# Performance work log

Measured on AMD Instinct MI355X. Metric: run time of the kernel, lower is better.

## Reference

```python
import jax, jax.numpy as jnp
import numpy as np

D_MODEL = 512
N_HEADS = 8
HEAD_DIM = D_MODEL // N_HEADS
B, T = 128, 256


def setup_inputs() -> dict:
    key = jax.random.key(0)
    ks = jax.random.split(key, 5)
    s = 1.0 / np.sqrt(D_MODEL)
    return {
        "x": jax.random.normal(ks[0], (B, T, D_MODEL), dtype=jnp.float32),
        "W_qkv": jax.random.uniform(ks[1], (D_MODEL, 3 * D_MODEL), jnp.float32, -s, s),
        "b_qkv": jax.random.uniform(ks[2], (3 * D_MODEL,), jnp.float32, -s, s),
        "W_out": jax.random.uniform(ks[3], (D_MODEL, D_MODEL), jnp.float32, -s, s),
        "b_out": jax.random.uniform(ks[4], (D_MODEL,), jnp.float32, -s, s),
    }


def reference(x, W_qkv, b_qkv, W_out, b_out):
    Bsz, Tlen, C = x.shape
    H, hd = N_HEADS, HEAD_DIM
    qkv = x @ W_qkv + b_qkv                       # [B,T,3C]
    qkv = qkv.reshape(Bsz, Tlen, 3, H, hd).transpose(2, 0, 3, 1, 4)  # [3,B,H,T,hd]
    q, k, v = qkv[0], qkv[1], qkv[2]
    att = jnp.einsum('bhtd,bhsd->bhts', q, k) * (1.0 / np.sqrt(hd))  # [B,H,T,T]
    causal = jnp.tril(jnp.ones((Tlen, Tlen), dtype=bool))
    att = jnp.where(causal, att, -jnp.inf)
    att = jax.nn.softmax(att, axis=-1)
    y = jnp.einsum('bhts,bhsd->bhtd', att, v)     # [B,H,T,hd]
    y = y.transpose(0, 2, 1, 3).reshape(Bsz, Tlen, C)
    return y @ W_out + b_out
```

## Files before the change

### kernel.cpp

```cpp
#include <hip/hip_runtime.h>
#include <hip/hip_bf16.h>

typedef __attribute__((ext_vector_type(4))) float f32x4;
typedef __attribute__((ext_vector_type(8))) short s16x8;
typedef unsigned short u16;

__device__ __forceinline__ u16 f2bf(float f) {
    union { float f; unsigned int u; } a; a.f = f;
    unsigned int u = a.u;
    unsigned int lsb = (u >> 16) & 1u;
    u += 0x7fffu + lsb;
    return (u16)(u >> 16);
}

__device__ __forceinline__ void gll16(const u16* g, u16* l) {
    __builtin_amdgcn_global_load_lds(
        (const __attribute__((address_space(1))) unsigned int*)g,
        (__attribute__((address_space(3))) unsigned int*)l, 16, 0, 0);
}


__global__ __launch_bounds__(256) void cvt_all_kernel(const float* __restrict__ x,
                                                      const float* __restrict__ W_qkv,
                                                      const float* __restrict__ W_out,
                                                      u16* __restrict__ xb,
                                                      u16* __restrict__ WqkvT,
                                                      u16* __restrict__ WoutT) {
    int bid = blockIdx.x;
    if (bid < 16384) {
        int i = bid * 256 + threadIdx.x;
        float4 v = ((const float4*)x)[i];
        ushort4 o;
        o.x = f2bf(v.x); o.y = f2bf(v.y); o.z = f2bf(v.z); o.w = f2bf(v.w);
        ((ushort4*)xb)[i] = o;
    } else if (bid < 16768) {
        int id = (bid - 16384) * 256 + threadIdx.x;
        int n = id % 1536, kg = id / 1536;
        union { u16 h[8]; int4 v; } o;
#pragma unroll
        for (int e = 0; e < 8; ++e) o.h[e] = f2bf(W_qkv[(kg * 8 + e) * 1536 + n]);
        *(int4*)&WqkvT[n * 512 + kg * 8] = o.v;
    } else {
        int id = (bid - 16768) * 256 + threadIdx.x;
        int n = id % 512, kg = id / 512;
        union { u16 h[8]; int4 v; } o;
#pragma unroll
        for (int e = 0; e < 8; ++e) o.h[e] = f2bf(W_out[(kg * 8 + e) * 512 + n]);
        *(int4*)&WoutT[n * 512 + kg * 8] = o.v;
    }
}


template<int K>
__device__ __forceinline__ void stage256(const u16* __restrict__ A, const u16* __restrict__ Bt,
                                         int m0, int n0, int kt, u16* As, u16* Bs) {
    const int lane = threadIdx.x & 63, w = threadIdx.x >> 6;
    const int lr = lane >> 3;
    const int lg = lane & 7;
    const int sgA = lg ^ lr;
#pragma unroll
    for (int j = 0; j < 4; ++j) {
        const int blk = w * 4 + j;
        gll16(&A[(m0 + blk * 8 + lr) * K + kt + sgA * 8], &As[blk * 512]);
    }
#pragma unroll
    for (int j = 0; j < 4; ++j) {
        const int blk = w * 4 + j;
        const int sgB = lg ^ ((2 * j + (lr >> 2)) & 7);
        gll16(&Bt[(n0 + blk * 8 + lr) * K + kt + sgB * 8], &Bs[blk * 512]);
    }
}

template<int K>
__device__ __forceinline__ void gemm_tile256(const u16* __restrict__ A, const u16* __restrict__ Bt,
                                             int m0, int n0,
                                             u16* As0, u16* Bs0, u16* As1, u16* Bs1,
                                             f32x4 (&acc)[8][4]) {
    const int lane = threadIdx.x & 63, li = lane & 15, quad = lane >> 4;
    const int w = threadIdx.x >> 6;
    const int wr = w >> 2, wc = w & 3;
    const int sw = li & 7;

    stage256<K>(A, Bt, m0, n0, 0, As0, Bs0);
    __syncthreads();

#pragma unroll
    for (int kt = 0; kt < K / 64; ++kt) {
        u16* Asc = (kt & 1) ? As1 : As0;
        u16* Bsc = (kt & 1) ? Bs1 : Bs0;
        if (kt + 1 < K / 64)
            stage256<K>(A, Bt, m0, n0, (kt + 1) * 64,
                        (kt & 1) ? As0 : As1, (kt & 1) ? Bs0 : Bs1);
#pragma unroll
        for (int kc = 0; kc < 2; ++kc) {
            s16x8 af[8], bf[4];
#pragma unroll
            for (int i = 0; i < 8; ++i)
                af[i] = *(const s16x8*)&Asc[(wr * 128 + i * 16 + li) * 64 + (((quad + kc * 4) ^ sw)) * 8];
#pragma unroll
            for (int j = 0; j < 4; ++j)
                bf[j] = *(const s16x8*)&Bsc[(wc * 64 + li * 4 + j) * 64 + (((quad + kc * 4) ^ sw)) * 8];
#pragma unroll
            for (int i = 0; i < 8; ++i)
#pragma unroll
                for (int j = 0; j < 4; ++j)
                    acc[i][j] = __builtin_amdgcn_mfma_f32_16x16x32_bf16(af[i], bf[j], acc[i][j], 0, 0, 0);
        }
        __syncthreads();
    }
}


__global__ __launch_bounds__(512, 2) void gemm_qkv_kernel(const u16* __restrict__ xb,
                                                          const u16* __restrict__ WqkvT,
                                                          const float* __restrict__ b_qkv,
                                                          u16* __restrict__ Qb, u16* __restrict__ Kb,
                                                          u16* __restrict__ Vtb) {
    __shared__ __align__(16) u16 S[69632];
    u16* As0 = S;          u16* Bs0 = S + 16384;
    u16* As1 = S + 32768;  u16* Bs1 = S + 49152;

    f32x4 acc[8][4];
#pragma unroll
    for (int i = 0; i < 8; ++i)
#pragma unroll
        for (int j = 0; j < 4; ++j) acc[i][j] = {0.f, 0.f, 0.f, 0.f};

    const int id = blockIdx.x, xcd = id & 7, slot = id >> 3;
    const int mt = xcd * 16 + slot / 6, nt = slot % 6;
    const int m0 = mt * 256, n0 = nt * 256;
    gemm_tile256<512>(xb, WqkvT, m0, n0, As0, Bs0, As1, Bs1, acc);

    const int lane = threadIdx.x & 63, li = lane & 15, quad = lane >> 4;
    const int w = threadIdx.x >> 6, wr = w >> 2, wc = w & 3;
    const int c0 = n0 + wc * 64;
    float4 b4 = *(const float4*)&b_qkv[c0 + li * 4];

    if (n0 < 1024) {
        const int which = c0 >> 9, hh = (c0 >> 6) & 7;
        u16* __restrict__ dst = which ? Kb : Qb;
#pragma unroll
        for (int i = 0; i < 8; ++i)
#pragma unroll
            for (int r = 0; r < 4; ++r) {
                int row = m0 + wr * 128 + i * 16 + quad * 4 + r;
                int bb = row >> 8, tt = row & 255;
                int bh = (bb * 8 + hh) << 14;
                ushort4 o;
                o.x = f2bf(acc[i][0][r] + b4.x); o.y = f2bf(acc[i][1][r] + b4.y);
                o.z = f2bf(acc[i][2][r] + b4.z); o.w = f2bf(acc[i][3][r] + b4.w);
                *(ushort4*)&dst[bh + tt * 64 + li * 4] = o;
            }
    } else {
        u16* Rw = S + w * 8704;
#pragma unroll
        for (int i = 0; i < 8; ++i)
#pragma unroll
            for (int r = 0; r < 4; ++r) {
                int rl = i * 16 + quad * 4 + r;
                ushort4 o;
                o.x = f2bf(acc[i][0][r] + b4.x); o.y = f2bf(acc[i][1][r] + b4.y);
                o.z = f2bf(acc[i][2][r] + b4.z); o.w = f2bf(acc[i][3][r] + b4.w);
                *(ushort4*)&Rw[rl * 68 + li * 4] = o;
            }
        __syncthreads();
        const int hh = ((n0 >> 6) + wc) & 7;
        const size_t bh = ((size_t)(mt * 8 + hh)) << 14;
#pragma unroll
        for (int c = 0; c < 16; ++c) {
            int g = c * 64 + lane;
            int group = g >> 8;
            int d = (g & 255) >> 2;
            int sl8 = (g & 3) * 8;
            union { u16 h[8]; int4 v; } o;
#pragma unroll
            for (int e = 0; e < 8; ++e) o.h[e] = Rw[(group * 32 + sl8 + e) * 68 + d];
            *(int4*)&Vtb[bh + (wr * 4 + group) * 2048 + d * 32 + sl8] = o.v;
        }
    }
}


__global__ __launch_bounds__(512, 2) void gemm_out_kernel(const u16* __restrict__ Yb,
                                                          const u16* __restrict__ WoutT,
                                                          const float* __restrict__ b_out,
                                                          float* __restrict__ out) {
    __shared__ __align__(16) u16 As0[256 * 64];
    __shared__ __align__(16) u16 Bs0[256 * 64];
    __shared__ __align__(16) u16 As1[256 * 64];
    __shared__ __align__(16) u16 Bs1[256 * 64];
    f32x4 acc[8][4];
#pragma unroll
    for (int i = 0; i < 8; ++i)
#pragma unroll
        for (int j = 0; j < 4; ++j) acc[i][j] = {0.f, 0.f, 0.f, 0.f};

    const int id = blockIdx.x, xcd = id & 7, slot = id >> 3;
    const int mt = xcd * 16 + (slot >> 1), nt = slot & 1;
    const int m0 = mt * 256, n0 = nt * 256;
    gemm_tile256<512>(Yb, WoutT, m0, n0, As0, Bs0, As1, Bs1, acc);

    const int lane = threadIdx.x & 63, li = lane & 15, quad = lane >> 4;
    const int w = threadIdx.x >> 6, wr = w >> 2, wc = w & 3;
    const int c0 = n0 + wc * 64;
    float4 b4 = *(const float4*)&b_out[c0 + li * 4];

#pragma unroll
    for (int i = 0; i < 8; ++i)
#pragma unroll
        for (int r = 0; r < 4; ++r) {
            int row = m0 + wr * 128 + i * 16 + quad * 4 + r;
            float4 o;
            o.x = acc[i][0][r] + b4.x; o.y = acc[i][1][r] + b4.y;
            o.z = acc[i][2][r] + b4.z; o.w = acc[i][3][r] + b4.w;
            *(float4*)&out[row * 512 + c0 + li * 4] = o;
        }
}


__global__ __launch_bounds__(256, 2) void attn_kernel(const u16* __restrict__ Qb,
                                                      const u16* __restrict__ Kb,
                                                      const u16* __restrict__ Vtb,
                                                      u16* __restrict__ Yb) {
    __shared__ __align__(16) u16 Ks[256 * 64];
    __shared__ __align__(16) u16 pl[4 * 2 * 16 * 40];

    const int tid = threadIdx.x, wave = tid >> 6, lane = tid & 63, li = lane & 15, quad = lane >> 4;
    const int bhid = blockIdx.x;
    const int b = bhid >> 3, h = bhid & 7;
    const int bh = bhid << 14;

    s16x8 qf0 = *(const s16x8*)&Qb[bh + (wave * 16 + li) * 64 + quad * 8];
    s16x8 qf1 = *(const s16x8*)&Qb[bh + (wave * 16 + li) * 64 + 32 + quad * 8];

    {
        const int lr = lane >> 3;
        const int sg = (lane & 7) ^ lr;
#pragma unroll
        for (int j = 0; j < 8; ++j) {
            int blk = wave * 8 + j;
            gll16(&Kb[bh + (blk * 8 + lr) * 64 + sg * 8], &Ks[blk * 512]);
        }
    }
    __syncthreads();

    u16* plw = &pl[wave * 1280];

    for (int p = 0; p < 4; ++p) {
        const int qt = p * 4 + wave;
        const int qrb = qt * 16;
        const int nst = qt + 1;

        f32x4 sacc[16];
#pragma unroll
        for (int st = 0; st < 16; ++st) sacc[st] = {0.f, 0.f, 0.f, 0.f};
        const int sw = li & 7;
#pragma unroll
        for (int g = 0; g < 4; ++g) {
            if (g * 4 < nst) {
                s16x8 kf[4][2];
#pragma unroll
                for (int t = 0; t < 4; ++t) {
                    if (g * 4 + t < nst) {
                        int rb = ((g * 4 + t) * 16 + li) * 64;
                        kf[t][0] = *(const s16x8*)&Ks[rb + ((quad    ) ^ sw) * 8];
                        kf[t][1] = *(const s16x8*)&Ks[rb + ((quad + 4) ^ sw) * 8];
                    }
                }
#pragma unroll
                for (int t = 0; t < 4; ++t) {
                    if (g * 4 + t < nst) {
                        sacc[g*4+t] = __builtin_amdgcn_mfma_f32_16x16x32_bf16(qf0, kf[t][0], sacc[g*4+t], 0, 0, 0);
                        sacc[g*4+t] = __builtin_amdgcn_mfma_f32_16x16x32_bf16(qf1, kf[t][1], sacc[g*4+t], 0, 0, 0);
                    }
                }
            }
        }

        s16x8 nqf0 = qf0, nqf1 = qf1;
        if (p < 3) {
            int nqrb = ((p + 1) * 4 + wave) * 16;
            nqf0 = *(const s16x8*)&Qb[bh + (nqrb + li) * 64 + quad * 8];
            nqf1 = *(const s16x8*)&Qb[bh + (nqrb + li) * 64 + 32 + quad * 8];
        }

        float mx[4] = {-3e38f, -3e38f, -3e38f, -3e38f};
#pragma unroll
        for (int st = 0; st < 16; ++st) {
            if (st < nst) {
                int sg2 = st * 16 + li;
#pragma unroll
                for (int r = 0; r < 4; ++r) {
                    int tg = qrb + quad * 4 + r;
                    float v = (sg2 <= tg) ? sacc[st][r] * 0.125f : -3e38f;
                    sacc[st][r] = v;
                    mx[r] = fmaxf(mx[r], v);
                }
            }
        }
#pragma unroll
        for (int d = 1; d < 16; d <<= 1)
#pragma unroll
            for (int r = 0; r < 4; ++r) mx[r] = fmaxf(mx[r], __shfl_xor(mx[r], d, 64));

        const int ns32 = (nst + 1) >> 1;
        float l[4] = {0.f, 0.f, 0.f, 0.f};
        f32x4 oacc[4];
#pragma unroll
        for (int dt = 0; dt < 4; ++dt) oacc[dt] = {0.f, 0.f, 0.f, 0.f};

        s16x8 vf[2][4];
#pragma unroll
        for (int dt = 0; dt < 4; ++dt)
            vf[0][dt] = *(const s16x8*)&Vtb[bh + (li * 4 + dt) * 32 + quad * 8];

#pragma unroll
        for (int c = 0; c < 8; ++c) {
            if (c < ns32) {
                if (c + 1 < ns32) {
#pragma unroll
                    for (int dt = 0; dt < 4; ++dt)
                        vf[(c + 1) & 1][dt] = *(const s16x8*)&Vtb[bh + (c + 1) * 2048 + (li * 4 + dt) * 32 + quad * 8];
                }
                u16* pb = plw + (c & 1) * 640;
#pragma unroll
                for (int half = 0; half < 2; ++half) {
                    int st = c * 2 + half;
#pragma unroll
                    for (int r = 0; r < 4; ++r) {
                        float e = (st < nst) ? __expf(sacc[st][r] - mx[r]) : 0.f;
                        l[r] += e;
                        pb[(quad * 4 + r) * 40 + half * 16 + li] = f2bf(e);
                    }
                }
                s16x8 pf = *(const s16x8*)&pb[li * 40 + quad * 8];
#pragma unroll
                for (int dt = 0; dt < 4; ++dt)
                    oacc[dt] = __builtin_amdgcn_mfma_f32_16x16x32_bf16(pf, vf[c & 1][dt], oacc[dt], 0, 0, 0);
            }
        }

#pragma unroll
        for (int d = 1; d < 16; d <<= 1)
#pragma unroll
            for (int r = 0; r < 4; ++r) l[r] += __shfl_xor(l[r], d, 64);

#pragma unroll
        for (int r = 0; r < 4; ++r) {
            int tg = qrb + quad * 4 + r;
            float inv = 1.0f / l[r];
            ushort4 o;
            o.x = f2bf(oacc[0][r] * inv); o.y = f2bf(oacc[1][r] * inv);
            o.z = f2bf(oacc[2][r] * inv); o.w = f2bf(oacc[3][r] * inv);
            *(ushort4*)&Yb[(b * 256 + tg) * 512 + h * 64 + li * 4] = o;
        }

        qf0 = nqf0; qf1 = nqf1;
    }
}


extern "C" void kernel_launch(void* const* d_in, const int* in_sizes, int n_in,
                              void* d_out, int out_size, void* d_ws, size_t ws_size,
                              hipStream_t stream) {
    const float* x     = (const float*)d_in[0];
    const float* W_qkv = (const float*)d_in[1];
    const float* b_qkv = (const float*)d_in[2];
    const float* W_out = (const float*)d_in[3];
    const float* b_out = (const float*)d_in[4];
    float* out = (float*)d_out;

    char* ws = (char*)d_ws;
    u16* Qb    = (u16*)(ws);
    u16* Kb    = (u16*)(ws + 33554432);
    u16* Vtb   = (u16*)(ws + 67108864);
    u16* WqkvT = (u16*)(ws + 100663296);
    u16* WoutT = (u16*)(ws + 102236160);
    u16* xb    = (u16*)(ws + 102760448);
    u16* Yb    = xb;
    if (ws_size < (size_t)136314880) return;

    cvt_all_kernel<<<16896, 256, 0, stream>>>(x, W_qkv, W_out, xb, WqkvT, WoutT);
    gemm_qkv_kernel<<<768, 512, 0, stream>>>(xb, WqkvT, b_qkv, Qb, Kb, Vtb);
    attn_kernel<<<1024, 256, 0, stream>>>(Qb, Kb, Vtb, Yb);
    gemm_out_kernel<<<256, 512, 0, stream>>>(Yb, WoutT, b_out, out);
}
```

Before: 263.0 us.

## Single-buffer GEMM LDS, halve out-GEMM tile, balance attention and drop softmax max

The shared GEMM tile drops double buffering, halving LDS, and launch bounds go to 4 blocks per CU so more blocks can be resident. The QKV epilogue transposes V in two halves to fit the smaller LDS. The output GEMM moves to 128x256 tiles with twice as many blocks. The attention kernel interleaves query tiles per wave to balance causal work, and removes the running-max subtraction in softmax, exponentiating scaled scores directly. That risks overflow for large logits and loses load/compute overlap in the GEMMs.

```diff
diff --git a/kernel.cpp b/kernel.cpp
--- a/kernel.cpp
+++ b/kernel.cpp
@@ -55,8 +55,7 @@
 __device__ __forceinline__ void stage256(const u16* __restrict__ A, const u16* __restrict__ Bt,
                                          int m0, int n0, int kt, u16* As, u16* Bs) {
     const int lane = threadIdx.x & 63, w = threadIdx.x >> 6;
-    const int lr = lane >> 3;
-    const int lg = lane & 7;
+    const int lr = lane >> 3, lg = lane & 7;
     const int sgA = lg ^ lr;
 #pragma unroll
     for (int j = 0; j < 4; ++j) {
@@ -71,35 +70,29 @@
     }
 }
 
+
 template<int K>
 __device__ __forceinline__ void gemm_tile256(const u16* __restrict__ A, const u16* __restrict__ Bt,
-                                             int m0, int n0,
-                                             u16* As0, u16* Bs0, u16* As1, u16* Bs1,
+                                             int m0, int n0, u16* As, u16* Bs,
                                              f32x4 (&acc)[8][4]) {
     const int lane = threadIdx.x & 63, li = lane & 15, quad = lane >> 4;
     const int w = threadIdx.x >> 6;
     const int wr = w >> 2, wc = w & 3;
     const int sw = li & 7;
 
-    stage256<K>(A, Bt, m0, n0, 0, As0, Bs0);
-    __syncthreads();
-
 #pragma unroll
     for (int kt = 0; kt < K / 64; ++kt) {
-        u16* Asc = (kt & 1) ? As1 : As0;
-        u16* Bsc = (kt & 1) ? Bs1 : Bs0;
-        if (kt + 1 < K / 64)
-            stage256<K>(A, Bt, m0, n0, (kt + 1) * 64,
-                        (kt & 1) ? As0 : As1, (kt & 1) ? Bs0 : Bs1);
+        stage256<K>(A, Bt, m0, n0, kt * 64, As, Bs);
+        __syncthreads();
 #pragma unroll
         for (int kc = 0; kc < 2; ++kc) {
             s16x8 af[8], bf[4];
 #pragma unroll
             for (int i = 0; i < 8; ++i)
-                af[i] = *(const s16x8*)&Asc[(wr * 128 + i * 16 + li) * 64 + (((quad + kc * 4) ^ sw)) * 8];
+                af[i] = *(const s16x8*)&As[(wr * 128 + i * 16 + li) * 64 + (((quad + kc * 4) ^ sw)) * 8];
 #pragma unroll
             for (int j = 0; j < 4; ++j)
-                bf[j] = *(const s16x8*)&Bsc[(wc * 64 + li * 4 + j) * 64 + (((quad + kc * 4) ^ sw)) * 8];
+                bf[j] = *(const s16x8*)&Bs[(wc * 64 + li * 4 + j) * 64 + (((quad + kc * 4) ^ sw)) * 8];
 #pragma unroll
             for (int i = 0; i < 8; ++i)
 #pragma unroll
@@ -111,14 +104,14 @@
 }
 
 
-__global__ __launch_bounds__(512, 2) void gemm_qkv_kernel(const u16* __restrict__ xb,
+__global__ __launch_bounds__(512, 4) void gemm_qkv_kernel(const u16* __restrict__ xb,
                                                           const u16* __restrict__ WqkvT,
                                                           const float* __restrict__ b_qkv,
                                                           u16* __restrict__ Qb, u16* __restrict__ Kb,
                                                           u16* __restrict__ Vtb) {
-    __shared__ __align__(16) u16 S[69632];
-    u16* As0 = S;          u16* Bs0 = S + 16384;
-    u16* As1 = S + 32768;  u16* Bs1 = S + 49152;
+    __shared__ __align__(16) u16 S[34816];
+    u16* As = S;
+    u16* Bs = S + 16384;
 
     f32x4 acc[8][4];
 #pragma unroll
@@ -129,7 +122,7 @@
     const int id = blockIdx.x, xcd = id & 7, slot = id >> 3;
     const int mt = xcd * 16 + slot / 6, nt = slot % 6;
     const int m0 = mt * 256, n0 = nt * 256;
-    gemm_tile256<512>(xb, WqkvT, m0, n0, As0, Bs0, As1, Bs1, acc);
+    gemm_tile256<512>(xb, WqkvT, m0, n0, As, Bs, acc);
 
     const int lane = threadIdx.x & 63, li = lane & 15, quad = lane >> 4;
     const int w = threadIdx.x >> 6, wr = w >> 2, wc = w & 3;
@@ -152,64 +145,99 @@
                 *(ushort4*)&dst[bh + tt * 64 + li * 4] = o;
             }
     } else {
-        u16* Rw = S + w * 8704;
-#pragma unroll
-        for (int i = 0; i < 8; ++i)
-#pragma unroll
-            for (int r = 0; r < 4; ++r) {
-                int rl = i * 16 + quad * 4 + r;
-                ushort4 o;
-                o.x = f2bf(acc[i][0][r] + b4.x); o.y = f2bf(acc[i][1][r] + b4.y);
-                o.z = f2bf(acc[i][2][r] + b4.z); o.w = f2bf(acc[i][3][r] + b4.w);
-                *(ushort4*)&Rw[rl * 68 + li * 4] = o;
-            }
-        __syncthreads();
         const int hh = ((n0 >> 6) + wc) & 7;
         const size_t bh = ((size_t)(mt * 8 + hh)) << 14;
-#pragma unroll
-        for (int c = 0; c < 16; ++c) {
-            int g = c * 64 + lane;
-            int group = g >> 8;
-            int d = (g & 255) >> 2;
-            int sl8 = (g & 3) * 8;
-            union { u16 h[8]; int4 v; } o;
-#pragma unroll
-            for (int e = 0; e < 8; ++e) o.h[e] = Rw[(group * 32 + sl8 + e) * 68 + d];
-            *(int4*)&Vtb[bh + (wr * 4 + group) * 2048 + d * 32 + sl8] = o.v;
-        }
-    }
-}
-
-
-__global__ __launch_bounds__(512, 2) void gemm_out_kernel(const u16* __restrict__ Yb,
+        u16* Rw = S + w * 4352;
+#pragma unroll
+        for (int h2 = 0; h2 < 2; ++h2) {
+#pragma unroll
+            for (int i = 0; i < 4; ++i)
+#pragma unroll
+                for (int r = 0; r < 4; ++r) {
+                    int ai = h2 * 4 + i;
+                    int rl = i * 16 + quad * 4 + r;
+                    ushort4 o;
+                    o.x = f2bf(acc[ai][0][r] + b4.x); o.y = f2bf(acc[ai][1][r] + b4.y);
+                    o.z = f2bf(acc[ai][2][r] + b4.z); o.w = f2bf(acc[ai][3][r] + b4.w);
+                    *(ushort4*)&Rw[rl * 68 + li * 4] = o;
+                }
+#pragma unroll
+            for (int c = 0; c < 8; ++c) {
+                int g = c * 64 + lane;
+                int group = g >> 8;
+                int d = (g & 255) >> 2;
+                int sl8 = (g & 3) * 8;
+                union { u16 h[8]; int4 v; } o;
+#pragma unroll
+                for (int e = 0; e < 8; ++e) o.h[e] = Rw[(group * 32 + sl8 + e) * 68 + d];
+                *(int4*)&Vtb[bh + (wr * 4 + h2 * 2 + group) * 2048 + d * 32 + sl8] = o.v;
+            }
+        }
+    }
+}
+
+
+__global__ __launch_bounds__(512, 4) void gemm_out_kernel(const u16* __restrict__ Yb,
                                                           const u16* __restrict__ WoutT,
                                                           const float* __restrict__ b_out,
                                                           float* __restrict__ out) {
-    __shared__ __align__(16) u16 As0[256 * 64];
-    __shared__ __align__(16) u16 Bs0[256 * 64];
-    __shared__ __align__(16) u16 As1[256 * 64];
-    __shared__ __align__(16) u16 Bs1[256 * 64];
-    f32x4 acc[8][4];
-#pragma unroll
-    for (int i = 0; i < 8; ++i)
+    __shared__ __align__(16) u16 As[8192];
+    __shared__ __align__(16) u16 Bs[16384];
+    f32x4 acc[4][4];
+#pragma unroll
+    for (int i = 0; i < 4; ++i)
 #pragma unroll
         for (int j = 0; j < 4; ++j) acc[i][j] = {0.f, 0.f, 0.f, 0.f};
 
     const int id = blockIdx.x, xcd = id & 7, slot = id >> 3;
-    const int mt = xcd * 16 + (slot >> 1), nt = slot & 1;
-    const int m0 = mt * 256, n0 = nt * 256;
-    gemm_tile256<512>(Yb, WoutT, m0, n0, As0, Bs0, As1, Bs1, acc);
+    const int mt = xcd * 32 + (slot >> 1), nt = slot & 1;
+    const int m0 = mt * 128, n0 = nt * 256;
 
     const int lane = threadIdx.x & 63, li = lane & 15, quad = lane >> 4;
     const int w = threadIdx.x >> 6, wr = w >> 2, wc = w & 3;
+    const int sw = li & 7;
+    const int lr = lane >> 3, lg = lane & 7;
+    const int sgA = lg ^ lr;
+
+#pragma unroll
+    for (int kt = 0; kt < 8; ++kt) {
+#pragma unroll
+        for (int j = 0; j < 2; ++j) {
+            const int blk = w * 2 + j;
+            gll16(&Yb[(m0 + blk * 8 + lr) * 512 + kt * 64 + sgA * 8], &As[blk * 512]);
+        }
+#pragma unroll
+        for (int j = 0; j < 4; ++j) {
+            const int blk = w * 4 + j;
+            const int sgB = lg ^ ((2 * j + (lr >> 2)) & 7);
+            gll16(&WoutT[(n0 + blk * 8 + lr) * 512 + kt * 64 + sgB * 8], &Bs[blk * 512]);
+        }
+        __syncthreads();
+#pragma unroll
+        for (int kc = 0; kc < 2; ++kc) {
+            s16x8 af[4], bf[4];
+#pragma unroll
+            for (int i = 0; i < 4; ++i)
+                af[i] = *(const s16x8*)&As[(wr * 64 + i * 16 + li) * 64 + (((quad + kc * 4) ^ sw)) * 8];
+#pragma unroll
+            for (int j = 0; j < 4; ++j)
+                bf[j] = *(const s16x8*)&Bs[(wc * 64 + li * 4 + j) * 64 + (((quad + kc * 4) ^ sw)) * 8];
+#pragma unroll
+            for (int i = 0; i < 4; ++i)
+#pragma unroll
+                for (int j = 0; j < 4; ++j)
+                    acc[i][j] = __builtin_amdgcn_mfma_f32_16x16x32_bf16(af[i], bf[j], acc[i][j], 0, 0, 0);
+        }
+        __syncthreads();
+    }
+
     const int c0 = n0 + wc * 64;
     float4 b4 = *(const float4*)&b_out[c0 + li * 4];
-
-#pragma unroll
-    for (int i = 0; i < 8; ++i)
+#pragma unroll
+    for (int i = 0; i < 4; ++i)
 #pragma unroll
         for (int r = 0; r < 4; ++r) {
-            int row = m0 + wr * 128 + i * 16 + quad * 4 + r;
+            int row = m0 + wr * 64 + i * 16 + quad * 4 + r;
             float4 o;
             o.x = acc[i][0][r] + b4.x; o.y = acc[i][1][r] + b4.y;
             o.z = acc[i][2][r] + b4.z; o.w = acc[i][3][r] + b4.w;
@@ -246,8 +274,9 @@
 
     u16* plw = &pl[wave * 1280];
 
+#pragma unroll
     for (int p = 0; p < 4; ++p) {
-        const int qt = p * 4 + wave;
+        const int qt = (p == 0) ? wave : (p == 1) ? (7 - wave) : (p == 2) ? (8 + wave) : (15 - wave);
         const int qrb = qt * 16;
         const int nst = qt + 1;
 
@@ -279,29 +308,11 @@
 
         s16x8 nqf0 = qf0, nqf1 = qf1;
         if (p < 3) {
-            int nqrb = ((p + 1) * 4 + wave) * 16;
+            int nqt = (p == 0) ? (7 - wave) : (p == 1) ? (8 + wave) : (15 - wave);
+            int nqrb = nqt * 16;
             nqf0 = *(const s16x8*)&Qb[bh + (nqrb + li) * 64 + quad * 8];
             nqf1 = *(const s16x8*)&Qb[bh + (nqrb + li) * 64 + 32 + quad * 8];
         }
-
-        float mx[4] = {-3e38f, -3e38f, -3e38f, -3e38f};
-#pragma unroll
-        for (int st = 0; st < 16; ++st) {
-            if (st < nst) {
-                int sg2 = st * 16 + li;
-#pragma unroll
-                for (int r = 0; r < 4; ++r) {
-                    int tg = qrb + quad * 4 + r;
-                    float v = (sg2 <= tg) ? sacc[st][r] * 0.125f : -3e38f;
-                    sacc[st][r] = v;
-                    mx[r] = fmaxf(mx[r], v);
-                }
-            }
-        }
-#pragma unroll
-        for (int d = 1; d < 16; d <<= 1)
-#pragma unroll
-            for (int r = 0; r < 4; ++r) mx[r] = fmaxf(mx[r], __shfl_xor(mx[r], d, 64));
 
         const int ns32 = (nst + 1) >> 1;
         float l[4] = {0.f, 0.f, 0.f, 0.f};
@@ -326,9 +337,11 @@
 #pragma unroll
                 for (int half = 0; half < 2; ++half) {
                     int st = c * 2 + half;
+                    int sg2 = st * 16 + li;
 #pragma unroll
                     for (int r = 0; r < 4; ++r) {
-                        float e = (st < nst) ? __expf(sacc[st][r] - mx[r]) : 0.f;
+                        int tg = qrb + quad * 4 + r;
+                        float e = (st < nst && sg2 <= tg) ? __expf(sacc[st][r] * 0.125f) : 0.f;
                         l[r] += e;
                         pb[(quad * 4 + r) * 40 + half * 16 + li] = f2bf(e);
                     }
@@ -383,5 +396,5 @@
     cvt_all_kernel<<<16896, 256, 0, stream>>>(x, W_qkv, W_out, xb, WqkvT, WoutT);
     gemm_qkv_kernel<<<768, 512, 0, stream>>>(xb, WqkvT, b_qkv, Qb, Kb, Vtb);
     attn_kernel<<<1024, 256, 0, stream>>>(Qb, Kb, Vtb, Yb);
-    gemm_out_kernel<<<256, 512, 0, stream>>>(Yb, WoutT, b_out, out);
-}
+    gemm_out_kernel<<<512, 512, 0, stream>>>(Yb, WoutT, b_out, out);
+}
```

New measurement: 628.2 us. 2.39x slower.
